# Kernel tuning notes

Measured on AMD Instinct MI355X. Metric: run time of the kernel, lower is better.

## Reference

```python
import math
import jax
import jax.numpy as jnp
import numpy as np

NUM_TOKENS = 8192
MODEL_DIM = 2048
NUM_EXPERTS = 64
CAPACITY_FACTOR = 1.0


def setup_inputs() -> dict:
    key = jax.random.key(0)
    k1, k2 = jax.random.split(key)
    x = jax.random.normal(k1, (NUM_TOKENS, MODEL_DIM), dtype=jnp.float32)
    # gate weight, torch Linear layout [num_experts, model_dim]
    wg = jax.random.normal(k2, (NUM_EXPERTS, MODEL_DIM), dtype=jnp.float32) / np.sqrt(MODEL_DIM).astype(np.float32)
    return {"x": x, "wg": wg}


def top2gating(logits, capacity_factor):
    s, e = logits.shape  # static under jit
    capacity = int(math.ceil(2 * s / e * capacity_factor))
    gates = jax.nn.softmax(logits, axis=1)  # [s, e]

    # top-1 expert
    indices1_s = jnp.argmax(gates, axis=1)
    mask1 = jax.nn.one_hot(indices1_s, e, dtype=jnp.int32)  # [s, e]

    # top-2 expert via gumbel-perturbed logits with expert-1 masked out
    gumbel = jax.random.gumbel(jax.random.key(42), logits.shape, dtype=logits.dtype)
    logits_w_noise = logits + gumbel
    logits_except1 = jnp.where(mask1.astype(bool), -jnp.inf, logits_w_noise)
    indices2_s = jnp.argmax(logits_except1, axis=1)
    mask2 = jax.nn.one_hot(indices2_s, e, dtype=jnp.int32)

    # positions within each expert's buffer (prefix sums over tokens)
    locations1 = jnp.cumsum(mask1, axis=0) - 1  # [s, e]
    locations2 = jnp.cumsum(mask2, axis=0) - 1
    locations2 = locations2 + jnp.sum(mask1, axis=0, keepdims=True)

    # load-balancing aux loss
    me = jnp.mean(gates, axis=0)
    ce = jnp.mean(mask1.astype(gates.dtype), axis=0)
    l_aux = jnp.mean(me * ce) * (e * e)

    # drop tokens beyond capacity
    mask1 = mask1 * (locations1 < capacity).astype(jnp.int32)
    mask2 = mask2 * (locations2 < capacity).astype(jnp.int32)

    locations1_s = jnp.sum(locations1 * mask1, axis=1)  # [s]
    locations2_s = jnp.sum(locations2 * mask2, axis=1)

    mask1_f = mask1.astype(gates.dtype)
    mask2_f = mask2.astype(gates.dtype)
    gates1_s = jnp.sum(gates * mask1_f, axis=1)  # [s]
    gates2_s = jnp.sum(gates * mask2_f, axis=1)
    denom_s = jnp.maximum(gates1_s + gates2_s, jnp.finfo(gates.dtype).eps)
    gates1_s = gates1_s / denom_s
    gates2_s = gates2_s / denom_s

    gates1 = gates1_s[:, None] * mask1_f  # [s, e]
    gates2 = gates2_s[:, None] * mask2_f

    locations1_sc = jax.nn.one_hot(locations1_s, capacity, dtype=gates.dtype)  # [s, c]
    locations2_sc = jax.nn.one_hot(locations2_s, capacity, dtype=gates.dtype)

    combine_weights = (gates1[:, :, None] * locations1_sc[:, None, :]
                       + gates2[:, :, None] * locations2_sc[:, None, :])  # [s, e, c]
    dispatch_mask = combine_weights.astype(bool)
    return l_aux, combine_weights, dispatch_mask


def reference(x, wg):
    logits = x @ wg.T  # [s, e]
    return top2gating(logits, CAPACITY_FACTOR)
```

## Files before the change

### kernel.cpp

```cpp
#include <hip/hip_runtime.h>
#include <hip/hip_bf16.h>
#include <stdint.h>

#define TOKENS 8192
#define DIM 2048
#define EXPERTS 64
#define CAP 256
#define COMB_ELEMS ((size_t)TOKENS * EXPERTS * CAP)
#define OUT_ELEMS (1 + 2 * COMB_ELEMS)

#define GEMM_BLOCKS 256
#define ZERO_BLOCKS 2048

typedef float f32x4 __attribute__((ext_vector_type(4)));

__device__ __forceinline__ void tf_round(uint32_t& a, uint32_t& b, int r) {
  a += b;
  b = (b << r) | (b >> (32 - r));
  b ^= a;
}

__device__ __forceinline__ void threefry2x32(uint32_t k0, uint32_t k1,
                                             uint32_t x0, uint32_t x1,
                                             uint32_t& o0, uint32_t& o1) {
  const uint32_t ks0 = k0, ks1 = k1, ks2 = k0 ^ k1 ^ 0x1BD11BDAu;
  x0 += ks0; x1 += ks1;
  tf_round(x0, x1, 13); tf_round(x0, x1, 15); tf_round(x0, x1, 26); tf_round(x0, x1, 6);
  x0 += ks1; x1 += ks2 + 1u;
  tf_round(x0, x1, 17); tf_round(x0, x1, 29); tf_round(x0, x1, 16); tf_round(x0, x1, 24);
  x0 += ks2; x1 += ks0 + 2u;
  tf_round(x0, x1, 13); tf_round(x0, x1, 15); tf_round(x0, x1, 26); tf_round(x0, x1, 6);
  x0 += ks0; x1 += ks1 + 3u;
  tf_round(x0, x1, 17); tf_round(x0, x1, 29); tf_round(x0, x1, 16); tf_round(x0, x1, 24);
  x0 += ks1; x1 += ks2 + 4u;
  tf_round(x0, x1, 13); tf_round(x0, x1, 15); tf_round(x0, x1, 26); tf_round(x0, x1, 6);
  x0 += ks2; x1 += ks0 + 5u;
  o0 = x0; o1 = x1;
}

__global__ __launch_bounds__(256) void k_fused(const float* __restrict__ x,
                                               const float* __restrict__ wg,
                                               float* __restrict__ out,
                                               int* __restrict__ e1, int* __restrict__ e2,
                                               float* __restrict__ g1, float* __restrict__ g2,
                                               float* __restrict__ gpart) {
  __shared__ float xs[32][33];
  __shared__ float wt[32][64];
  __shared__ float gpl[4][64];

  const int tid = threadIdx.x;

  if (blockIdx.x >= GEMM_BLOCKS) {
    f32x4* o4 = reinterpret_cast<f32x4*>(out);
    const int zb = blockIdx.x - GEMM_BLOCKS;
    const size_t stride = (size_t)ZERO_BLOCKS * 256;
    size_t i = (size_t)zb * 256 + tid;
    const f32x4 z = {0.f, 0.f, 0.f, 0.f};
#pragma unroll 4
    for (int it = 0; it < 64; ++it) {
      __builtin_nontemporal_store(z, &o4[i]);
      __builtin_nontemporal_store(z, &o4[i + stride]);
      i += 2 * stride;
    }
    if (zb == 0 && tid == 0) out[2 * COMB_ELEMS] = 0.f;
    return;
  }

  const int tok0 = blockIdx.x * 32;
  const int e0 = (tid & 15) * 4;
  const int t0 = (tid >> 4) * 2;

  const int xr = tid >> 3;
  const int xc = (tid & 7) << 2;
  const int wr = tid >> 2;
  const int wc = (tid & 3) << 3;

  const float* xp = x + (size_t)(tok0 + xr) * DIM + xc;
  const float* wp = wg + (size_t)wr * DIM + wc;

  float4 xv  = *reinterpret_cast<const float4*>(xp);
  float4 wv0 = *reinterpret_cast<const float4*>(wp);
  float4 wv1 = *reinterpret_cast<const float4*>(wp + 4);

  float acc[2][4] = {{0.f, 0.f, 0.f, 0.f}, {0.f, 0.f, 0.f, 0.f}};

  for (int k0 = 0; k0 < DIM; k0 += 32) {
    *reinterpret_cast<float4*>(&xs[xr][xc]) = xv;
    wt[wc + 0][wr] = wv0.x; wt[wc + 1][wr] = wv0.y;
    wt[wc + 2][wr] = wv0.z; wt[wc + 3][wr] = wv0.w;
    wt[wc + 4][wr] = wv1.x; wt[wc + 5][wr] = wv1.y;
    wt[wc + 6][wr] = wv1.z; wt[wc + 7][wr] = wv1.w;
    __syncthreads();
    if (k0 + 32 < DIM) {
      xv  = *reinterpret_cast<const float4*>(xp + k0 + 32);
      wv0 = *reinterpret_cast<const float4*>(wp + k0 + 32);
      wv1 = *reinterpret_cast<const float4*>(wp + k0 + 36);
    }
#pragma unroll
    for (int kk = 0; kk < 32; ++kk) {
      const float4 b = *reinterpret_cast<const float4*>(&wt[kk][e0]);
      const float a0 = xs[t0][kk];
      const float a1 = xs[t0 + 1][kk];
      acc[0][0] = fmaf(a0, b.x, acc[0][0]);
      acc[0][1] = fmaf(a0, b.y, acc[0][1]);
      acc[0][2] = fmaf(a0, b.z, acc[0][2]);
      acc[0][3] = fmaf(a0, b.w, acc[0][3]);
      acc[1][0] = fmaf(a1, b.x, acc[1][0]);
      acc[1][1] = fmaf(a1, b.y, acc[1][1]);
      acc[1][2] = fmaf(a1, b.z, acc[1][2]);
      acc[1][3] = fmaf(a1, b.w, acc[1][3]);
    }
    __syncthreads();
  }

#pragma unroll
  for (int i = 0; i < 2; ++i)
    *reinterpret_cast<float4*>(&wt[t0 + i][e0]) =
        make_float4(acc[i][0], acc[i][1], acc[i][2], acc[i][3]);
  __syncthreads();

  const int w = tid >> 6;
  const int lane = tid & 63;
  float colsum = 0.f;
  for (int lt = w * 8; lt < w * 8 + 8; ++lt) {
    const int t = tok0 + lt;
    const float logit = wt[lt][lane];

    float m = logit;
#pragma unroll
    for (int off = 32; off > 0; off >>= 1) m = fmaxf(m, __shfl_xor(m, off));
    const float ex = expf(logit - m);
    float s = ex;
#pragma unroll
    for (int off = 32; off > 0; off >>= 1) s += __shfl_xor(s, off);
    const float gate = ex / s;
    colsum += gate;

    float v1 = logit; int i1 = lane;
#pragma unroll
    for (int off = 32; off > 0; off >>= 1) {
      const float ov = __shfl_xor(v1, off);
      const int oi = __shfl_xor(i1, off);
      if (ov > v1 || (ov == v1 && oi < i1)) { v1 = ov; i1 = oi; }
    }

    const uint32_t i_flat = (uint32_t)t * 64u + (uint32_t)lane;
    uint32_t b0, b1;
    threefry2x32(0u, 42u, 0u, i_flat, b0, b1);
    const uint32_t bits = b0 ^ b1;
    float u = __uint_as_float((bits >> 9) | 0x3f800000u) - 1.0f;
    u += 1.17549435e-38f;
    const float gum = -logf(-logf(u));
    const float noisy = (lane == i1) ? -__builtin_inff() : (logit + gum);

    float v2 = noisy; int i2 = lane;
#pragma unroll
    for (int off = 32; off > 0; off >>= 1) {
      const float ov = __shfl_xor(v2, off);
      const int oi = __shfl_xor(i2, off);
      if (ov > v2 || (ov == v2 && oi < i2)) { v2 = ov; i2 = oi; }
    }

    const float gate1 = __shfl(gate, i1);
    const float gate2 = __shfl(gate, i2);
    if (lane == 0) { e1[t] = i1; e2[t] = i2; g1[t] = gate1; g2[t] = gate2; }
  }
  gpl[w][lane] = colsum;
  __syncthreads();
  if (w == 0)
    gpart[(size_t)blockIdx.x * 64 + lane] =
        (gpl[0][lane] + gpl[1][lane]) + (gpl[2][lane] + gpl[3][lane]);
}

__global__ __launch_bounds__(256) void k_scan(const int* __restrict__ e1,
    const int* __restrict__ e2, const float* __restrict__ gpart,
    int* __restrict__ loc1, int* __restrict__ loc2,
    int* __restrict__ counts1, float* __restrict__ gsum) {
  const int e = blockIdx.x;
  const int tid = threadIdx.x;
  const int lane = tid & 63;
  const int w = tid >> 6;
  __shared__ int wt1[32][4], wt2[32][4];
  __shared__ int pre1[32][4], pre2[32][4];
  __shared__ int c1tot;
  __shared__ float gw[4];

  float gp = gpart[(size_t)tid * 64 + e];
#pragma unroll
  for (int off = 32; off > 0; off >>= 1) gp += __shfl_xor(gp, off);
  if (lane == 0) gw[w] = gp;

  const uint64_t ltm = (lane == 0) ? 0ull : ((~0ull) >> (64 - lane));

  int r1[32], r2[32];
#pragma unroll
  for (int s = 0; s < 32; ++s) {
    const int t = s * 256 + tid;
    const bool q1 = (e1[t] == e);
    const bool q2 = (e2[t] == e);
    const uint64_t m1 = __ballot(q1);
    const uint64_t m2 = __ballot(q2);
    r1[s] = q1 ? (int)__popcll(m1 & ltm) + 1 : 0;
    r2[s] = q2 ? (int)__popcll(m2 & ltm) + 1 : 0;
    if (lane == 0) { wt1[s][w] = (int)__popcll(m1); wt2[s][w] = (int)__popcll(m2); }
  }
  __syncthreads();

  if (tid == 0) gsum[e] = (gw[0] + gw[1]) + (gw[2] + gw[3]);

  if (w == 0) {
    {
      int va = wt1[lane >> 2][lane & 3];
      int vb = wt1[(64 + lane) >> 2][(64 + lane) & 3];
      int sa = va, sb = vb;
#pragma unroll
      for (int d = 1; d < 64; d <<= 1) {
        const int t1 = __shfl_up(sa, d);
        const int t2 = __shfl_up(sb, d);
        if (lane >= d) { sa += t1; sb += t2; }
      }
      const int tot_a = __shfl(sa, 63);
      pre1[lane >> 2][lane & 3] = sa - va;
      pre1[(64 + lane) >> 2][(64 + lane) & 3] = tot_a + sb - vb;
      if (lane == 63) c1tot = tot_a + sb;
    }
    {
      int va = wt2[lane >> 2][lane & 3];
      int vb = wt2[(64 + lane) >> 2][(64 + lane) & 3];
      int sa = va, sb = vb;
#pragma unroll
      for (int d = 1; d < 64; d <<= 1) {
        const int t1 = __shfl_up(sa, d);
        const int t2 = __shfl_up(sb, d);
        if (lane >= d) { sa += t1; sb += t2; }
      }
      const int tot_a = __shfl(sa, 63);
      pre2[lane >> 2][lane & 3] = sa - va;
      pre2[(64 + lane) >> 2][(64 + lane) & 3] = tot_a + sb - vb;
    }
  }
  __syncthreads();

  const int c1 = c1tot;
  if (tid == 0) counts1[e] = c1;

#pragma unroll
  for (int s = 0; s < 32; ++s) {
    const int t = s * 256 + tid;
    if (r1[s]) loc1[t] = pre1[s][w] + r1[s] - 1;
    if (r2[s]) loc2[t] = c1 + pre2[s][w] + r2[s] - 1;
  }
}

__global__ __launch_bounds__(256) void k_scatter(const int* __restrict__ e1,
    const int* __restrict__ e2, const float* __restrict__ g1,
    const float* __restrict__ g2, const int* __restrict__ loc1,
    const int* __restrict__ loc2, const float* __restrict__ gsum,
    const int* __restrict__ counts1, float* __restrict__ out) {
  const int tid = threadIdx.x;
  if (blockIdx.x == 0 && tid < 64) {
    float v = gsum[tid] * (float)counts1[tid];
#pragma unroll
    for (int off = 32; off > 0; off >>= 1) v += __shfl_xor(v, off);
    if (tid == 0) out[0] = v * (1.0f / 1048576.0f);
  }
  const int t = blockIdx.x * 256 + tid;
  const int a = e1[t], b = e2[t];
  const int l1 = loc1[t], l2 = loc2[t];
  const bool k1 = l1 < CAP;
  const bool k2 = l2 < CAP;
  const float ga = k1 ? g1[t] : 0.f;
  const float gb = k2 ? g2[t] : 0.f;
  const float denom = fmaxf(ga + gb, 1.1920929e-07f);
  float* __restrict__ combine = out + 1;
  float* __restrict__ dispatch = out + 1 + COMB_ELEMS;
  if (k1) {
    const size_t idx = ((size_t)t * EXPERTS + a) * CAP + l1;
    combine[idx] = ga / denom;
    dispatch[idx] = 1.0f;
  }
  if (k2) {
    const size_t idx = ((size_t)t * EXPERTS + b) * CAP + l2;
    combine[idx] = gb / denom;
    dispatch[idx] = 1.0f;
  }
}

extern "C" void kernel_launch(void* const* d_in, const int* in_sizes, int n_in,
                              void* d_out, int out_size, void* d_ws, size_t ws_size,
                              hipStream_t stream) {
  const float* x = (const float*)d_in[0];
  const float* wg = (const float*)d_in[1];
  float* out = (float*)d_out;

  int*   e1      = (int*)d_ws;
  int*   e2      = e1 + TOKENS;
  int*   loc1    = e2 + TOKENS;
  int*   loc2    = loc1 + TOKENS;
  int*   counts1 = loc2 + TOKENS;
  float* g1      = (float*)(counts1 + 64);
  float* g2      = g1 + TOKENS;
  float* gsum    = g2 + TOKENS;
  float* gpart   = gsum + 64;

  k_fused<<<GEMM_BLOCKS + ZERO_BLOCKS, 256, 0, stream>>>(x, wg, out, e1, e2, g1, g2, gpart);
  k_scan<<<EXPERTS, 256, 0, stream>>>(e1, e2, gpart, loc1, loc2, counts1, gsum);
  k_scatter<<<TOKENS / 256, 256, 0, stream>>>(e1, e2, g1, g2, loc1, loc2, gsum, counts1, out);
}
```

Measured before the change: 1.144 ms.

## Fuse zero-fill and scatter into one dense output-fill pass after scan

Removes the zero-fill from the GEMM/gating kernel and replaces the separate sparse scatter kernel with a single dense fill kernel. That kernel computes every output element directly, writing either zero, the gate weight or the dispatch flag, so the large output buffer is written once instead of zeroed and then partially overwritten. The trade-off is that the ~1 GB write no longer overlaps the GEMM, and each element now does per-token index decoding and loads (cached) inside the store loop.

```diff
diff --git a/kernel.cpp b/kernel.cpp
--- a/kernel.cpp
+++ b/kernel.cpp
@@ -10,7 +10,7 @@
 #define OUT_ELEMS (1 + 2 * COMB_ELEMS)
 
 #define GEMM_BLOCKS 256
-#define ZERO_BLOCKS 2048
+#define FILL_BLOCKS 2048
 
 typedef float f32x4 __attribute__((ext_vector_type(4)));
 
@@ -38,34 +38,16 @@
   o0 = x0; o1 = x1;
 }
 
-__global__ __launch_bounds__(256) void k_fused(const float* __restrict__ x,
-                                               const float* __restrict__ wg,
-                                               float* __restrict__ out,
-                                               int* __restrict__ e1, int* __restrict__ e2,
-                                               float* __restrict__ g1, float* __restrict__ g2,
-                                               float* __restrict__ gpart) {
+__global__ __launch_bounds__(256) void k_gemm_gate(const float* __restrict__ x,
+    const float* __restrict__ wg,
+    int* __restrict__ e1, int* __restrict__ e2,
+    float* __restrict__ g1, float* __restrict__ g2,
+    float* __restrict__ gpart) {
   __shared__ float xs[32][33];
   __shared__ float wt[32][64];
   __shared__ float gpl[4][64];
 
   const int tid = threadIdx.x;
-
-  if (blockIdx.x >= GEMM_BLOCKS) {
-    f32x4* o4 = reinterpret_cast<f32x4*>(out);
-    const int zb = blockIdx.x - GEMM_BLOCKS;
-    const size_t stride = (size_t)ZERO_BLOCKS * 256;
-    size_t i = (size_t)zb * 256 + tid;
-    const f32x4 z = {0.f, 0.f, 0.f, 0.f};
-#pragma unroll 4
-    for (int it = 0; it < 64; ++it) {
-      __builtin_nontemporal_store(z, &o4[i]);
-      __builtin_nontemporal_store(z, &o4[i + stride]);
-      i += 2 * stride;
-    }
-    if (zb == 0 && tid == 0) out[2 * COMB_ELEMS] = 0.f;
-    return;
-  }
-
   const int tok0 = blockIdx.x * 32;
   const int e0 = (tid & 15) * 4;
   const int t0 = (tid >> 4) * 2;
@@ -252,37 +234,65 @@
   }
 }
 
-__global__ __launch_bounds__(256) void k_scatter(const int* __restrict__ e1,
-    const int* __restrict__ e2, const float* __restrict__ g1,
-    const float* __restrict__ g2, const int* __restrict__ loc1,
-    const int* __restrict__ loc2, const float* __restrict__ gsum,
+__global__ __launch_bounds__(256) void k_fill(const int* __restrict__ e1,
+    const int* __restrict__ e2, const int* __restrict__ l1,
+    const int* __restrict__ l2, const float* __restrict__ g1,
+    const float* __restrict__ g2, const float* __restrict__ gsum,
     const int* __restrict__ counts1, float* __restrict__ out) {
   const int tid = threadIdx.x;
-  if (blockIdx.x == 0 && tid < 64) {
+  const int bid = blockIdx.x;
+
+  float laux = 0.f;
+  if (bid == 0 && tid < 64) {
     float v = gsum[tid] * (float)counts1[tid];
 #pragma unroll
     for (int off = 32; off > 0; off >>= 1) v += __shfl_xor(v, off);
-    if (tid == 0) out[0] = v * (1.0f / 1048576.0f);
-  }
-  const int t = blockIdx.x * 256 + tid;
-  const int a = e1[t], b = e2[t];
-  const int l1 = loc1[t], l2 = loc2[t];
-  const bool k1 = l1 < CAP;
-  const bool k2 = l2 < CAP;
-  const float ga = k1 ? g1[t] : 0.f;
-  const float gb = k2 ? g2[t] : 0.f;
-  const float denom = fmaxf(ga + gb, 1.1920929e-07f);
-  float* __restrict__ combine = out + 1;
-  float* __restrict__ dispatch = out + 1 + COMB_ELEMS;
-  if (k1) {
-    const size_t idx = ((size_t)t * EXPERTS + a) * CAP + l1;
-    combine[idx] = ga / denom;
-    dispatch[idx] = 1.0f;
-  }
-  if (k2) {
-    const size_t idx = ((size_t)t * EXPERTS + b) * CAP + l2;
-    combine[idx] = gb / denom;
-    dispatch[idx] = 1.0f;
+    laux = v * (1.0f / 1048576.0f);
+  }
+
+  f32x4* o4 = reinterpret_cast<f32x4*>(out);
+  size_t ch = (size_t)bid * 32768 + tid;
+  for (int it = 0; it < 128; ++it, ch += 256) {
+    const size_t g0 = ch * 4;
+    f32x4 v = {0.f, 0.f, 0.f, 0.f};
+#pragma unroll
+    for (int k = 0; k < 4; ++k) {
+      const size_t g = g0 + k;
+      float val = 0.f;
+      if (g == 0) {
+        val = laux;
+      } else {
+        const size_t gm = g - 1;
+        const bool disp = gm >= COMB_ELEMS;
+        const uint32_t idx = (uint32_t)(disp ? gm - COMB_ELEMS : gm);
+        const int t = idx >> 14;
+        const int e = (idx >> 8) & 63;
+        const int c = idx & 255;
+        const int a = e1[t], b = e2[t];
+        const int la = l1[t], lb = l2[t];
+        const bool h1 = (e == a) & (c == la);
+        const bool h2 = (e == b) & (c == lb);
+        if (h1 | h2) {
+          if (disp) {
+            val = 1.0f;
+          } else {
+            const float ga = (la < CAP) ? g1[t] : 0.f;
+            const float gb = (lb < CAP) ? g2[t] : 0.f;
+            const float denom = fmaxf(ga + gb, 1.1920929e-07f);
+            val = (h1 ? ga : gb) / denom;
+          }
+        }
+      }
+      v[k] = val;
+    }
+    __builtin_nontemporal_store(v, &o4[ch]);
+  }
+
+  if (bid == 0 && tid == 0) {
+    const uint32_t idx = (uint32_t)(COMB_ELEMS - 1);
+    const int t = idx >> 14, e = (idx >> 8) & 63, c = idx & 255;
+    const bool hit = (e == e1[t] && c == l1[t]) || (e == e2[t] && c == l2[t]);
+    out[2 * COMB_ELEMS] = hit ? 1.0f : 0.f;
   }
 }
 
@@ -303,7 +313,7 @@
   float* gsum    = g2 + TOKENS;
   float* gpart   = gsum + 64;
 
-  k_fused<<<GEMM_BLOCKS + ZERO_BLOCKS, 256, 0, stream>>>(x, wg, out, e1, e2, g1, g2, gpart);
+  k_gemm_gate<<<GEMM_BLOCKS, 256, 0, stream>>>(x, wg, e1, e2, g1, g2, gpart);
   k_scan<<<EXPERTS, 256, 0, stream>>>(e1, e2, gpart, loc1, loc2, counts1, gsum);
-  k_scatter<<<TOKENS / 256, 256, 0, stream>>>(e1, e2, g1, g2, loc1, loc2, gsum, counts1, out);
-}
+  k_fill<<<FILL_BLOCKS, 256, 0, stream>>>(e1, e2, loc1, loc2, g1, g2, gsum, counts1, out);
+}
```

Measured after the change: 1.156 ms. No clear change (+1.0%).
